# Optimization experiments

Hardware: AMD Instinct MI355X
Metric: run time of the kernel (lower is better)

The kernel has to match this reference:

```python
import jax, jax.numpy as jnp
import numpy as np

B, H, IN, OUT, T = 1024, 1024, 512, 8192, 15
EPS = 1e-5


def setup_inputs() -> dict:
    key = jax.random.key(0)
    ks = jax.random.split(key, 20)
    s = 0.02
    d = {
        'z': jax.random.normal(ks[0], (B, H), jnp.float32),
        'input_length': T,
        # ConvTranspose1d weights, torch layout [in, out, k] == jax 'IOH'
        'cw1': jax.random.normal(ks[1], (H, H, 3), jnp.float32) * s,
        'cb1': jax.random.normal(ks[2], (H,), jnp.float32) * s,
        'cw2': jax.random.normal(ks[3], (H, H, 3), jnp.float32) * s,
        'cb2': jax.random.normal(ks[4], (H,), jnp.float32) * s,
        'cw3': jax.random.normal(ks[5], (H, H, 3), jnp.float32) * s,
        'cb3': jax.random.normal(ks[6], (H,), jnp.float32) * s,
        # BatchNorm1d (eval mode: running stats)
        'bn1_g': jnp.ones((H,), jnp.float32), 'bn1_b': jnp.zeros((H,), jnp.float32),
        'bn1_m': jax.random.normal(ks[7], (H,), jnp.float32) * 0.1,
        'bn1_v': jax.random.uniform(ks[8], (H,), jnp.float32, 0.5, 1.5),
        'bn2_g': jnp.ones((H,), jnp.float32), 'bn2_b': jnp.zeros((H,), jnp.float32),
        'bn2_m': jax.random.normal(ks[9], (H,), jnp.float32) * 0.1,
        'bn2_v': jax.random.uniform(ks[10], (H,), jnp.float32, 0.5, 1.5),
        # GRUCell: weight_ih [3H, IN+H], weight_hh [3H, H]
        'w_ih': jax.random.normal(ks[11], (3 * H, IN + H), jnp.float32) * s,
        'w_hh': jax.random.normal(ks[12], (3 * H, H), jnp.float32) * s,
        'b_ih': jax.random.normal(ks[13], (3 * H,), jnp.float32) * s,
        'b_hh': jax.random.normal(ks[14], (3 * H,), jnp.float32) * s,
        # Linears (torch layout [out_features, in_features])
        'h2x_w': jax.random.normal(ks[15], (IN, H), jnp.float32) * s,
        'h2x_b': jax.random.normal(ks[16], (IN,), jnp.float32) * s,
        'dec2out_w': jax.random.normal(ks[17], (OUT, H), jnp.float32) * s,
        'dec2out_b': jnp.zeros((OUT,), jnp.float32),
        'out_w': jax.random.normal(ks[18], (OUT, H), jnp.float32) * s,
        'out_b': jnp.zeros((OUT,), jnp.float32),
    }
    return d


def _conv_t(x, w, b):
    # x: [B, C, L] ; torch ConvTranspose1d(k=3, s=2, pad=0): out L -> 2L+1
    y = jax.lax.conv_transpose(x, w, strides=(2,), padding='VALID',
                               dimension_numbers=('NCH', 'IOH', 'NCH'),
                               transpose_kernel=True)
    return y + b[None, :, None]


def _bn(x, g, bta, m, v):
    inv = g / jnp.sqrt(v + EPS)
    return (x - m[None, :, None]) * inv[None, :, None] + bta[None, :, None]


def reference(z, input_length, cw1, cb1, cw2, cb2, cw3, cb3,
              bn1_g, bn1_b, bn1_m, bn1_v, bn2_g, bn2_b, bn2_m, bn2_v,
              w_ih, w_hh, b_ih, b_hh, h2x_w, h2x_b,
              dec2out_w, dec2out_b, out_w, out_b):
    b = z.shape[0]
    # conv-transpose context: [B, H, 1] -> [B, H, 15]
    dec = z[:, :, None]
    dec = _bn(jax.nn.elu(_conv_t(dec, cw1, cb1)), bn1_g, bn1_b, bn1_m, bn1_v)
    dec = _bn(jax.nn.elu(_conv_t(dec, cw2, cb2)), bn2_g, bn2_b, bn2_m, bn2_v)
    dec = _conv_t(dec, cw3, cb3)
    dec_tbh = jnp.transpose(dec, (2, 0, 1))[:input_length]  # [T, B, H]

    inp0 = jnp.full((b, IN), float(OUT - 2), z.dtype)

    def step(carry, dec_t):
        h, inp = carry
        x = jnp.concatenate([inp, dec_t], axis=1)         # [B, IN+H]
        gi = x @ w_ih.T + b_ih
        gh = h @ w_hh.T + b_hh
        ir, iz, inn = jnp.split(gi, 3, axis=1)
        hr, hz, hn = jnp.split(gh, 3, axis=1)
        r = jax.nn.sigmoid(ir + hr)
        zg = jax.nn.sigmoid(iz + hz)
        n = jnp.tanh(inn + r * hn)
        h_new = (1.0 - zg) * n + zg * h
        inp_new = jax.nn.relu(h_new @ h2x_w.T + h2x_b)    # eval-mode branch
        return (h_new, inp_new), h_new

    (_, _), hs = jax.lax.scan(step, (z, inp0), dec_tbh)   # hs: [T, B, H]

    dec_flat = dec_tbh.reshape(-1, H)
    out_flat = hs.reshape(-1, H)
    dec_o = dec_flat @ dec2out_w.T + dec2out_b            # [T*B, OUT]
    output = out_flat @ out_w.T + out_b                   # [T*B, OUT]
    return output, dec_o
```

## Files before the change

kernel.cpp:

```cpp
#include <hip/hip_runtime.h>
#include <math.h>


#define HD    1024
#define BATCH 1024
#define IND   512
#define OUTD  8192
#define TSTEPS 15
#define EPSV  1e-5f

typedef unsigned short u16;
typedef __attribute__((ext_vector_type(8))) short bf16x8;
typedef __attribute__((ext_vector_type(8))) unsigned short u16x8;
typedef __attribute__((ext_vector_type(4))) unsigned short u16x4;
typedef __attribute__((ext_vector_type(4))) float f32x4;

__device__ __forceinline__ u16 f2b(float f) {
    union { float f; unsigned u; } x; x.f = f;
    unsigned r = x.u + 0x7fffu + ((x.u >> 16) & 1u);
    return (u16)(r >> 16);
}
__device__ __forceinline__ float b2f(u16 v) {
    union { unsigned u; float f; } x; x.u = ((unsigned)v) << 16; return x.f;
}

typedef __attribute__((address_space(1))) const void gas_t;
typedef __attribute__((address_space(3))) void las_t;
__device__ __forceinline__ void gload_lds16(const u16* g, u16* l) {
    __builtin_amdgcn_global_load_lds((gas_t*)g, (las_t*)l, 16, 0, 0);
}

template<int EPI, bool WF32, bool WB16>
__device__ __forceinline__ void gemm_tile128(
    u16* As, u16* Bs,
    int bm, int bn,
    int K1, const u16* A1, int lda1, const u16* B1, int ldb1,
    int K2, const u16* A2, int lda2, const u16* B2, int ldb2,
    const float* bias,
    const float* bng, const float* bnb, const float* bnm, const float* bnv,
    float* Cf, u16* Cb, int ldc)
{
    const int tid  = threadIdx.x;
    const int lane = tid & 63;
    const int w    = tid >> 6;
    const int wr   = w >> 1, wc = w & 1;
    const int r_in = lane >> 2;
    const int c_in = (lane & 3) * 8;

    f32x4 acc[4][4];
#pragma unroll
    for (int m = 0; m < 4; ++m)
#pragma unroll
        for (int n = 0; n < 4; ++n) acc[m][n] = (f32x4){0.f, 0.f, 0.f, 0.f};

#pragma unroll 1
    for (int pair = 0; pair < 2; ++pair) {
        const int K = pair ? K2 : K1;
        if (K == 0) continue;
        const int lda = pair ? lda2 : lda1;
        const int ldb = pair ? ldb2 : ldb1;
        const u16* Ag = (pair ? A2 : A1) + (size_t)bm * lda;
        const u16* Bg = (pair ? B2 : B1) + (size_t)bn * ldb;

        for (int k0 = 0; k0 < K; k0 += 32) {
#pragma unroll
            for (int i = 0; i < 2; ++i) {
                gload_lds16(Ag + (size_t)(i * 64 + w * 16 + r_in) * lda + k0 + c_in,
                            &As[i * 2048 + w * 512]);
                gload_lds16(Bg + (size_t)(i * 64 + w * 16 + r_in) * ldb + k0 + c_in,
                            &Bs[i * 2048 + w * 512]);
            }
            __syncthreads();

            const int fr = lane & 15;
            const int fk = (lane >> 4) * 8;
            bf16x8 av[4], bv[4];
#pragma unroll
            for (int m = 0; m < 4; ++m)
                av[m] = *(const bf16x8*)&As[(wr * 64 + m * 16 + fr) * 32 + fk];
#pragma unroll
            for (int n = 0; n < 4; ++n)
                bv[n] = *(const bf16x8*)&Bs[(wc * 64 + n * 16 + fr) * 32 + fk];
#pragma unroll
            for (int m = 0; m < 4; ++m)
#pragma unroll
                for (int n = 0; n < 4; ++n)
                    acc[m][n] = __builtin_amdgcn_mfma_f32_16x16x32_bf16(
                                    av[m], bv[n], acc[m][n], 0, 0, 0);
            __syncthreads();
        }
    }

    const int col_l = lane & 15;
    const int row_h = (lane >> 4) * 4;
#pragma unroll
    for (int m = 0; m < 4; ++m) {
#pragma unroll
        for (int j = 0; j < 4; ++j) {
            const int row = bm + wr * 64 + m * 16 + row_h + j;
#pragma unroll
            for (int n = 0; n < 4; ++n) {
                const int col = bn + wc * 64 + n * 16 + col_l;
                float v = acc[m][n][j] + bias[col];
                if (EPI == 1) {
                    float e = v > 0.f ? v : expm1f(v);
                    float sc = bng[col] * rsqrtf(bnv[col] + EPSV);
                    v = (e - bnm[col]) * sc + bnb[col];
                }
                if (WF32) Cf[(size_t)row * ldc + col] = v;
                if (WB16) Cb[(size_t)row * ldc + col] = f2b(v);
            }
        }
    }
}

__device__ __forceinline__ void proj_rider(u16* sm, int g,
    const u16* A, const u16* B, const float* bias, float* C)
{
    gemm_tile128<0, true, false>(sm, sm + 4096,
        (g >> 6) * 128, (g & 63) * 128,
        HD, A, HD, B, HD, 0, nullptr, 0, nullptr, 0,
        bias, nullptr, nullptr, nullptr, nullptr, C, nullptr, OUTD);
}

__device__ __forceinline__ void gdec_rider(u16* sm, int t, int g,
    const u16* dec3b, const u16* wihb, const float* b_ih, u16* gdecb)
{
    const int row = g / 24, col = g - row * 24;
    gemm_tile128<0, false, true>(sm, sm + 4096,
        row * 128, col * 128,
        HD, dec3b + (size_t)t * BATCH * HD, HD, wihb + IND, IND + HD,
        0, nullptr, 0, nullptr, 0,
        b_ih, nullptr, nullptr, nullptr, nullptr,
        nullptr, gdecb + (size_t)t * BATCH * 3 * HD, 3 * HD);
}

__launch_bounds__(256)
__global__ void gdec_head(const u16* __restrict__ dec3b, const u16* __restrict__ wihb,
                          const float* __restrict__ b_ih, u16* __restrict__ gdecb)
{
    __shared__ __align__(16) u16 sm[8192];
    const int bid = blockIdx.x;
    if (bid < 192) gdec_rider(sm, 0, bid, dec3b, wihb, b_ih, gdecb);
    else           gdec_rider(sm, 1, bid - 192, dec3b, wihb, b_ih, gdecb);
}

template<int EPI>
__launch_bounds__(256)
__global__ void conv_gemm(int Lin, const u16* X, const u16* W, const float* bias,
                          const float* bng, const float* bnb, const float* bnm, const float* bnv,
                          u16* Y)
{
    __shared__ __align__(16) u16 sm[8192];
    const int t = blockIdx.z;
    int l0 = 0, k0 = 0, l1 = 0, k1 = 0, cnt = 0;
    for (int l = 0; l < Lin; ++l) {
        int k = t - 2 * l;
        if (k >= 0 && k < 3) { if (!cnt) { l0 = l; k0 = k; } else { l1 = l; k1 = k; } ++cnt; }
    }
    const size_t BH = (size_t)BATCH * HD, HH = (size_t)HD * HD;
    gemm_tile128<EPI, false, true>(sm, sm + 4096,
        blockIdx.y * 128, blockIdx.x * 128,
        HD, X + l0 * BH, HD, W + k0 * HH, HD,
        cnt > 1 ? HD : 0, X + l1 * BH, HD, W + k1 * HH, HD,
        bias, bng, bnb, bnm, bnv, nullptr, Y + (size_t)t * BH, HD);
}

#define KTILE(Ag, lda_, Bg, ldb_, k0_, ACC2)                                      \
  {                                                                               \
    const int k0 = (k0_);                                                         \
    gload_lds16((Ag) + (size_t)(tid >> 2) * (lda_) + k0 + (tid & 3) * 8,          \
                &As[tid * 8]);                                                    \
    _Pragma("unroll")                                                             \
    for (int i_ = 0; i_ < 3; ++i_) {                                              \
      const int u_ = tid + i_ * 256;                                              \
      gload_lds16((Bg) + (size_t)((u_ >> 8) * HD + bn + ((u_ & 255) >> 2)) * (ldb_)\
                       + k0 + (u_ & 3) * 8,                                       \
                  &Bs[u_ * 8]);                                                   \
    }                                                                             \
    __syncthreads();                                                              \
    {                                                                             \
      bf16x8 av0 = *(const bf16x8*)&As[(wr * 32 + fr) * 32 + fk];                 \
      bf16x8 av1 = *(const bf16x8*)&As[(wr * 32 + 16 + fr) * 32 + fk];            \
      _Pragma("unroll")                                                           \
      for (int n_ = 0; n_ < 2; ++n_) {                                            \
        const int bo = (wc * 32 + n_ * 16 + fr) * 32 + fk;                        \
        bf16x8 bv = *(const bf16x8*)&Bs[bo];                                      \
        ar[0][n_] = __builtin_amdgcn_mfma_f32_16x16x32_bf16(av0, bv, ar[0][n_], 0, 0, 0); \
        ar[1][n_] = __builtin_amdgcn_mfma_f32_16x16x32_bf16(av1, bv, ar[1][n_], 0, 0, 0); \
        bv = *(const bf16x8*)&Bs[2048 + bo];                                      \
        az[0][n_] = __builtin_amdgcn_mfma_f32_16x16x32_bf16(av0, bv, az[0][n_], 0, 0, 0); \
        az[1][n_] = __builtin_amdgcn_mfma_f32_16x16x32_bf16(av1, bv, az[1][n_], 0, 0, 0); \
        bv = *(const bf16x8*)&Bs[4096 + bo];                                      \
        ACC2[0][n_] = __builtin_amdgcn_mfma_f32_16x16x32_bf16(av0, bv, ACC2[0][n_], 0, 0, 0); \
        ACC2[1][n_] = __builtin_amdgcn_mfma_f32_16x16x32_bf16(av1, bv, ACC2[1][n_], 0, 0, 0); \
      }                                                                           \
    }                                                                             \
    __syncthreads();                                                              \
  }

__launch_bounds__(256)
__global__ void gih_cell(int t,
    const u16* __restrict__ inpb,  const u16* __restrict__ wih,
    const u16* __restrict__ hbp,   const u16* __restrict__ whh,
    const u16* __restrict__ gdecb, const float* __restrict__ extra0,
    const float* __restrict__ b_hh, const float* __restrict__ hp,
    float* __restrict__ hf, u16* __restrict__ hsbt,
    const u16* __restrict__ dec3b, const u16* __restrict__ d2owb,
    const float* __restrict__ d2ob, float* __restrict__ out1,
    const float* __restrict__ b_ih)
{
    __shared__ __align__(16) u16 sm[8192];
    const int bid = blockIdx.x;
    const int tid = threadIdx.x, l = tid & 63, w = tid >> 6;
    const int wr = w >> 1, wc = w & 1;
    const int fr = l & 15, fk = (l >> 4) * 8;

    if (bid >= 256) {
        int rid = bid - 256;
        if (t <= 12) {
            if (rid < 192) {
                gdec_rider(sm, t + 2, rid, dec3b, wih, b_ih, (u16*)gdecb);
                return;
            }
            rid -= 192;
        }
        proj_rider(sm, t * 512 + rid, dec3b, d2owb, d2ob, out1);
        return;
    }

    u16* As = sm;
    u16* Bs = sm + 2048;
    const int bm = (bid >> 4) * 64;
    const int bn = (bid & 15) * 64;

    f32x4 ar[2][2], az[2][2], ain[2][2], ahn[2][2];
#pragma unroll
    for (int m = 0; m < 2; ++m)
#pragma unroll
        for (int n = 0; n < 2; ++n) {
            ar[m][n] = (f32x4){0.f, 0.f, 0.f, 0.f};
            az[m][n] = (f32x4){0.f, 0.f, 0.f, 0.f};
            ain[m][n] = (f32x4){0.f, 0.f, 0.f, 0.f};
            ahn[m][n] = (f32x4){0.f, 0.f, 0.f, 0.f};
        }

    const u16* Ah = hbp + (size_t)bm * HD;
    const u16* Ai = inpb + (size_t)bm * IND;
    for (int kt = 0; kt < 32; ++kt)
        KTILE(Ah, HD, whh, HD, kt * 32, ahn);
    if (t > 0)
        for (int kt = 0; kt < 16; ++kt)
            KTILE(Ai, IND, wih, (IND + HD), kt * 32, ain);

    const u16* gdect = gdecb + (size_t)t * BATCH * 3 * HD;
    const int rh = (l >> 4) * 4;
#pragma unroll
    for (int m = 0; m < 2; ++m)
#pragma unroll
        for (int n = 0; n < 2; ++n)
#pragma unroll
            for (int j = 0; j < 4; ++j) {
                const int R = bm + wr * 32 + m * 16 + rh + j;
                const int C = bn + wc * 32 + n * 16 + fr;
                const size_t g3 = (size_t)R * (3 * HD);
                float gr  = ar[m][n][j] + b2f(gdect[g3 + C])      + b_hh[C];
                float gz  = az[m][n][j] + b2f(gdect[g3 + HD + C]) + b_hh[HD + C];
                float gin = ain[m][n][j] + b2f(gdect[g3 + 2 * HD + C]);
                float ghn = ahn[m][n][j] + b_hh[2 * HD + C];
                if (extra0) {
                    gr  += extra0[C];
                    gz  += extra0[HD + C];
                    gin += extra0[2 * HD + C];
                }
                const float rg = 1.f / (1.f + expf(-gr));
                const float zg = 1.f / (1.f + expf(-gz));
                const float nn = tanhf(gin + rg * ghn);
                const float h  = (1.f - zg) * nn + zg * hp[(size_t)R * HD + C];
                hf[(size_t)R * HD + C] = h;
                hsbt[(size_t)R * HD + C] = f2b(h);
            }
}

__launch_bounds__(256)
__global__ void h2x_k(int t,
    const u16* __restrict__ hbp, const u16* __restrict__ wx,
    const float* __restrict__ xb, u16* __restrict__ inp,
    const u16* __restrict__ hsb, const u16* __restrict__ outwb,
    const float* __restrict__ outb, float* __restrict__ out0)
{
    __shared__ __align__(16) u16 sm[8192];
    const int bid = blockIdx.x;
    const int tid = threadIdx.x, l = tid & 63, w = tid >> 6;
    const int wr = w >> 1, wc = w & 1;
    const int fr = l & 15, fk = (l >> 4) * 8;

    if (bid >= 128) {
        proj_rider(sm, (t - 1) * 512 + (bid - 128), hsb, outwb, outb, out0);
        return;
    }

    u16* As = sm;
    u16* Bs = sm + 2048;
    const int bm = (bid >> 3) * 64;
    const int bn = (bid & 7) * 64;

    f32x4 acc[2][2];
#pragma unroll
    for (int m = 0; m < 2; ++m)
#pragma unroll
        for (int n = 0; n < 2; ++n) acc[m][n] = (f32x4){0.f, 0.f, 0.f, 0.f};
    const u16* Ag = hbp + (size_t)bm * HD;
    const u16* Bg = wx + (size_t)bn * HD;
    for (int kt = 0; kt < 32; ++kt) {
        const int k0 = kt * 32;
        gload_lds16(Ag + (size_t)(tid >> 2) * HD + k0 + (tid & 3) * 8, &As[tid * 8]);
        gload_lds16(Bg + (size_t)(tid >> 2) * HD + k0 + (tid & 3) * 8, &Bs[tid * 8]);
        __syncthreads();
        bf16x8 av0 = *(const bf16x8*)&As[(wr * 32 + fr) * 32 + fk];
        bf16x8 av1 = *(const bf16x8*)&As[(wr * 32 + 16 + fr) * 32 + fk];
#pragma unroll
        for (int n = 0; n < 2; ++n) {
            bf16x8 bv = *(const bf16x8*)&Bs[(wc * 32 + n * 16 + fr) * 32 + fk];
            acc[0][n] = __builtin_amdgcn_mfma_f32_16x16x32_bf16(av0, bv, acc[0][n], 0, 0, 0);
            acc[1][n] = __builtin_amdgcn_mfma_f32_16x16x32_bf16(av1, bv, acc[1][n], 0, 0, 0);
        }
        __syncthreads();
    }
    const int rh = (l >> 4) * 4;
#pragma unroll
    for (int m = 0; m < 2; ++m)
#pragma unroll
        for (int n = 0; n < 2; ++n)
#pragma unroll
            for (int j = 0; j < 4; ++j) {
                const int R = bm + wr * 32 + m * 16 + rh + j;
                const int C = bn + wc * 32 + n * 16 + fr;
                inp[(size_t)R * IND + C] = f2b(fmaxf(acc[m][n][j] + xb[C], 0.f));
            }
}

__launch_bounds__(256)
__global__ void proj_k(int g0, const u16* __restrict__ A, const u16* __restrict__ B,
                       const float* __restrict__ bias, float* __restrict__ C)
{
    __shared__ __align__(16) u16 sm[8192];
    proj_rider(sm, g0 + blockIdx.x, A, B, bias, C);
}

__global__ void pack_w3(const float* __restrict__ c1, const float* __restrict__ c2,
                        const float* __restrict__ c3, u16* __restrict__ p1,
                        u16* __restrict__ p2, u16* __restrict__ p3)
{
    __shared__ float lds[768];
    const float* cw = blockIdx.y == 0 ? c1 : (blockIdx.y == 1 ? c2 : c3);
    u16* wp = blockIdx.y == 0 ? p1 : (blockIdx.y == 1 ? p2 : p3);
    const int o = blockIdx.x, t = threadIdx.x;
    const float* src = cw + (size_t)o * (HD * 3);
    for (int i0 = 0; i0 < HD; i0 += 256) {
#pragma unroll
        for (int r = 0; r < 3; ++r) lds[t + 256 * r] = src[i0 * 3 + t + 256 * r];
        __syncthreads();
#pragma unroll
        for (int k = 0; k < 3; ++k)
            wp[(size_t)k * HD * HD + (size_t)o * HD + i0 + t] = f2b(lds[t * 3 + k]);
        __syncthreads();
    }
}

__global__ void cvt_all(const float* s0, u16* d0, int n0,
                        const float* s1, u16* d1, int n1,
                        const float* s2, u16* d2, int n2,
                        const float* s3, u16* d3, int n3,
                        const float* s4, u16* d4, int n4,
                        const float* s5, u16* d5, int n5)
{
    const float* s; u16* d; int n;
    switch (blockIdx.y) {
        case 0:  s = s0; d = d0; n = n0; break;
        case 1:  s = s1; d = d1; n = n1; break;
        case 2:  s = s2; d = d2; n = n2; break;
        case 3:  s = s3; d = d3; n = n3; break;
        case 4:  s = s4; d = d4; n = n4; break;
        default: s = s5; d = d5; n = n5; break;
    }
    int i = (blockIdx.x * 256 + threadIdx.x) * 8;
    if (i >= n) return;
    float4 a = *(const float4*)(s + i);
    float4 b = *(const float4*)(s + i + 4);
    u16x8 o;
    o[0] = f2b(a.x); o[1] = f2b(a.y); o[2] = f2b(a.z); o[3] = f2b(a.w);
    o[4] = f2b(b.x); o[5] = f2b(b.y); o[6] = f2b(b.z); o[7] = f2b(b.w);
    *(u16x8*)(d + i) = o;
}

__global__ void ext0_k(const float* __restrict__ w_ih, float* __restrict__ e0)
{
    const int j = blockIdx.x, lane = threadIdx.x;
    float s = 0.f;
    for (int k = lane; k < IND; k += 64) s += w_ih[(size_t)j * (IND + HD) + k];
    for (int off = 32; off; off >>= 1) s += __shfl_down(s, off);
    if (lane == 0) e0[j] = 8190.f * s;
}

extern "C" void kernel_launch(void* const* d_in, const int* in_sizes, int n_in,
                              void* d_out, int out_size, void* d_ws, size_t ws_size,
                              hipStream_t stream)
{
    (void)in_sizes; (void)n_in; (void)out_size; (void)ws_size;

    const float* z    = (const float*)d_in[0];
    const float* cw1  = (const float*)d_in[2];
    const float* cb1  = (const float*)d_in[3];
    const float* cw2  = (const float*)d_in[4];
    const float* cb2  = (const float*)d_in[5];
    const float* cw3  = (const float*)d_in[6];
    const float* cb3  = (const float*)d_in[7];
    const float* bn1g = (const float*)d_in[8];
    const float* bn1b = (const float*)d_in[9];
    const float* bn1m = (const float*)d_in[10];
    const float* bn1v = (const float*)d_in[11];
    const float* bn2g = (const float*)d_in[12];
    const float* bn2b = (const float*)d_in[13];
    const float* bn2m = (const float*)d_in[14];
    const float* bn2v = (const float*)d_in[15];
    const float* w_ih = (const float*)d_in[16];
    const float* w_hh = (const float*)d_in[17];
    const float* b_ih = (const float*)d_in[18];
    const float* b_hh = (const float*)d_in[19];
    const float* h2xw = (const float*)d_in[20];
    const float* h2xb = (const float*)d_in[21];
    const float* d2ow = (const float*)d_in[22];
    const float* d2ob = (const float*)d_in[23];
    const float* outw = (const float*)d_in[24];
    const float* outb = (const float*)d_in[25];

    const size_t HH = (size_t)HD * HD, BH = (size_t)BATCH * HD;
    const size_t B3H = (size_t)BATCH * 3 * HD;

    u16* wsb = (u16*)d_ws;
    size_t off = 0;
    auto A16 = [&](size_t n) { u16* p = wsb + off; off += n; return p; };
    u16* wp1   = A16(3 * HH);
    u16* wp2   = A16(3 * HH);
    u16* wp3   = A16(3 * HH);
    u16* wihb  = A16((size_t)3 * HD * (IND + HD));
    u16* whhb  = A16(3 * HH);
    u16* h2xbw = A16((size_t)IND * HD);
    u16* outwb = A16((size_t)OUTD * HD);
    u16* d2owb = A16((size_t)OUTD * HD);
    u16* zb    = A16(BH);
    u16* decab = A16(3 * BH);
    u16* decbb = A16(7 * BH);
    u16* dec3b = A16(15 * BH);
    u16* hsb   = A16(15 * BH);
    u16* inpb  = A16((size_t)BATCH * IND);
    u16* gdecb = A16((size_t)TSTEPS * B3H);
    float* wsf = (float*)(wsb + ((off + 1) & ~(size_t)1));
    size_t foff = 0;
    auto A32 = [&](size_t n) { float* p = wsf + foff; foff += n; return p; };
    float* h0f   = A32(BH);
    float* h1f   = A32(BH);
    float* extra0= A32(3 * HD);

    pack_w3<<<dim3(HD, 3), 256, 0, stream>>>(cw1, cw2, cw3, wp1, wp2, wp3);
    cvt_all<<<dim3(4096, 6), 256, 0, stream>>>(
        z, zb, (int)BH,
        w_ih, wihb, 3 * HD * (IND + HD),
        w_hh, whhb, (int)(3 * HH),
        h2xw, h2xbw, IND * HD,
        outw, outwb, OUTD * HD,
        d2ow, d2owb, OUTD * HD);
    ext0_k<<<3 * HD, 64, 0, stream>>>(w_ih, extra0);

    conv_gemm<1><<<dim3(8, 8, 3), 256, 0, stream>>>(1, zb, wp1, cb1,
        bn1g, bn1b, bn1m, bn1v, decab);
    conv_gemm<1><<<dim3(8, 8, 7), 256, 0, stream>>>(3, decab, wp2, cb2,
        bn2g, bn2b, bn2m, bn2v, decbb);
    conv_gemm<0><<<dim3(8, 8, 15), 256, 0, stream>>>(7, decbb, wp3, cb3,
        nullptr, nullptr, nullptr, nullptr, dec3b);

    gdec_head<<<384, 256, 0, stream>>>(dec3b, wihb, b_ih, gdecb);

    float* out0 = (float*)d_out;
    float* out1 = out0 + (size_t)TSTEPS * BATCH * OUTD;
    for (int t = 0; t < TSTEPS; ++t) {
        const u16* hbp   = t ? hsb + (size_t)(t - 1) * BH : zb;
        const float* hpf = (t == 0) ? z : (((t - 1) & 1) ? h1f : h0f);
        float* hwf = (t & 1) ? h1f : h0f;
        if (t > 0)
            h2x_k<<<640, 256, 0, stream>>>(t, hbp, h2xbw, h2xb, inpb,
                hsb, outwb, outb, out0);
        const int ggrid = (t <= 12) ? 960 : 768;
        gih_cell<<<ggrid, 256, 0, stream>>>(t,
            inpb, wihb, hbp, whhb, gdecb,
            t ? nullptr : extra0, b_hh, hpf, hwf, hsb + (size_t)t * BH,
            dec3b, d2owb, d2ob, out1, b_ih);
    }
    proj_k<<<512, 256, 0, stream>>>(14 * 512, hsb, outwb, outb, out0);
}
```

Before: 1.486 ms.

## Double-buffer LDS tiles in GRU gate and h2x GEMM loops

Replaces the load-sync-compute-sync K loop in the gih_cell and h2x_k kernels with a two-stage LDS ping-pong. The next K tile's global-to-LDS loads are issued before the current tile's MFMAs, with explicit vmcnt waits and raw s_barrier. The goal is to hide global load latency inside these per-timestep recurrent kernels. It doubles shared memory for those blocks, which may lower occupancy for the rider blocks that share the kernel, and it relies on manual waitcnt counts being correct.

```diff
diff --git a/kernel.cpp b/kernel.cpp
--- a/kernel.cpp
+++ b/kernel.cpp
@@ -166,37 +166,25 @@
         bias, bng, bnb, bnm, bnv, nullptr, Y + (size_t)t * BH, HD);
 }
 
-#define KTILE(Ag, lda_, Bg, ldb_, k0_, ACC2)                                      \
+#define GIH_MMA(TGT)                                                              \
   {                                                                               \
-    const int k0 = (k0_);                                                         \
-    gload_lds16((Ag) + (size_t)(tid >> 2) * (lda_) + k0 + (tid & 3) * 8,          \
-                &As[tid * 8]);                                                    \
+    const u16* as = &As[buf * 2048];                                              \
+    const u16* bs = &Bs[buf * 6144];                                              \
+    bf16x8 av0 = *(const bf16x8*)&as[(wr * 32 + fr) * 32 + fk];                   \
+    bf16x8 av1 = *(const bf16x8*)&as[(wr * 32 + 16 + fr) * 32 + fk];              \
     _Pragma("unroll")                                                             \
-    for (int i_ = 0; i_ < 3; ++i_) {                                              \
-      const int u_ = tid + i_ * 256;                                              \
-      gload_lds16((Bg) + (size_t)((u_ >> 8) * HD + bn + ((u_ & 255) >> 2)) * (ldb_)\
-                       + k0 + (u_ & 3) * 8,                                       \
-                  &Bs[u_ * 8]);                                                   \
+    for (int n_ = 0; n_ < 2; ++n_) {                                              \
+      const int bo = (wc * 32 + n_ * 16 + fr) * 32 + fk;                          \
+      bf16x8 bv = *(const bf16x8*)&bs[bo];                                        \
+      ar[0][n_] = __builtin_amdgcn_mfma_f32_16x16x32_bf16(av0, bv, ar[0][n_], 0, 0, 0); \
+      ar[1][n_] = __builtin_amdgcn_mfma_f32_16x16x32_bf16(av1, bv, ar[1][n_], 0, 0, 0); \
+      bv = *(const bf16x8*)&bs[2048 + bo];                                        \
+      az[0][n_] = __builtin_amdgcn_mfma_f32_16x16x32_bf16(av0, bv, az[0][n_], 0, 0, 0); \
+      az[1][n_] = __builtin_amdgcn_mfma_f32_16x16x32_bf16(av1, bv, az[1][n_], 0, 0, 0); \
+      bv = *(const bf16x8*)&bs[4096 + bo];                                        \
+      TGT[0][n_] = __builtin_amdgcn_mfma_f32_16x16x32_bf16(av0, bv, TGT[0][n_], 0, 0, 0); \
+      TGT[1][n_] = __builtin_amdgcn_mfma_f32_16x16x32_bf16(av1, bv, TGT[1][n_], 0, 0, 0); \
     }                                                                             \
-    __syncthreads();                                                              \
-    {                                                                             \
-      bf16x8 av0 = *(const bf16x8*)&As[(wr * 32 + fr) * 32 + fk];                 \
-      bf16x8 av1 = *(const bf16x8*)&As[(wr * 32 + 16 + fr) * 32 + fk];            \
-      _Pragma("unroll")                                                           \
-      for (int n_ = 0; n_ < 2; ++n_) {                                            \
-        const int bo = (wc * 32 + n_ * 16 + fr) * 32 + fk;                        \
-        bf16x8 bv = *(const bf16x8*)&Bs[bo];                                      \
-        ar[0][n_] = __builtin_amdgcn_mfma_f32_16x16x32_bf16(av0, bv, ar[0][n_], 0, 0, 0); \
-        ar[1][n_] = __builtin_amdgcn_mfma_f32_16x16x32_bf16(av1, bv, ar[1][n_], 0, 0, 0); \
-        bv = *(const bf16x8*)&Bs[2048 + bo];                                      \
-        az[0][n_] = __builtin_amdgcn_mfma_f32_16x16x32_bf16(av0, bv, az[0][n_], 0, 0, 0); \
-        az[1][n_] = __builtin_amdgcn_mfma_f32_16x16x32_bf16(av1, bv, az[1][n_], 0, 0, 0); \
-        bv = *(const bf16x8*)&Bs[4096 + bo];                                      \
-        ACC2[0][n_] = __builtin_amdgcn_mfma_f32_16x16x32_bf16(av0, bv, ACC2[0][n_], 0, 0, 0); \
-        ACC2[1][n_] = __builtin_amdgcn_mfma_f32_16x16x32_bf16(av1, bv, ACC2[1][n_], 0, 0, 0); \
-      }                                                                           \
-    }                                                                             \
-    __syncthreads();                                                              \
   }
 
 __launch_bounds__(256)
@@ -210,7 +198,7 @@
     const float* __restrict__ d2ob, float* __restrict__ out1,
     const float* __restrict__ b_ih)
 {
-    __shared__ __align__(16) u16 sm[8192];
+    __shared__ __align__(16) u16 sm[16384];
     const int bid = blockIdx.x;
     const int tid = threadIdx.x, l = tid & 63, w = tid >> 6;
     const int wr = w >> 1, wc = w & 1;
@@ -230,7 +218,7 @@
     }
 
     u16* As = sm;
-    u16* Bs = sm + 2048;
+    u16* Bs = sm + 4096;
     const int bm = (bid >> 4) * 64;
     const int bn = (bid & 15) * 64;
 
@@ -247,11 +235,37 @@
 
     const u16* Ah = hbp + (size_t)bm * HD;
     const u16* Ai = inpb + (size_t)bm * IND;
-    for (int kt = 0; kt < 32; ++kt)
-        KTILE(Ah, HD, whh, HD, kt * 32, ahn);
-    if (t > 0)
-        for (int kt = 0; kt < 16; ++kt)
-            KTILE(Ai, IND, wih, (IND + HD), kt * 32, ain);
+    const int NT = (t > 0) ? 48 : 32;
+
+    auto stage = [&](int buf, int idx) {
+        const u16* Ag; int lda; const u16* Bg; int ldb; int k0;
+        if (idx < 32) { Ag = Ah; lda = HD;  Bg = whh; ldb = HD;       k0 = idx * 32; }
+        else          { Ag = Ai; lda = IND; Bg = wih; ldb = IND + HD; k0 = (idx - 32) * 32; }
+        gload_lds16(Ag + (size_t)(tid >> 2) * lda + k0 + (tid & 3) * 8,
+                    &As[buf * 2048 + tid * 8]);
+#pragma unroll
+        for (int i_ = 0; i_ < 3; ++i_) {
+            const int u_ = tid + i_ * 256;
+            gload_lds16(Bg + (size_t)((u_ >> 8) * HD + bn + ((u_ & 255) >> 2)) * ldb
+                           + k0 + (u_ & 3) * 8,
+                        &Bs[buf * 6144 + u_ * 8]);
+        }
+    };
+
+    stage(0, 0);
+#pragma unroll 1
+    for (int idx = 0; idx < NT; ++idx) {
+        const int buf = idx & 1;
+        if (idx + 1 < NT) {
+            stage(buf ^ 1, idx + 1);
+            asm volatile("s_waitcnt vmcnt(4)" ::: "memory");
+        } else {
+            asm volatile("s_waitcnt vmcnt(0)" ::: "memory");
+        }
+        __builtin_amdgcn_s_barrier();
+        if (idx < 32) { GIH_MMA(ahn); } else { GIH_MMA(ain); }
+        __builtin_amdgcn_s_barrier();
+    }
 
     const u16* gdect = gdecb + (size_t)t * BATCH * 3 * HD;
     const int rh = (l >> 4) * 4;
@@ -301,7 +315,7 @@
     }
 
     u16* As = sm;
-    u16* Bs = sm + 2048;
+    u16* Bs = sm + 4096;
     const int bm = (bid >> 3) * 64;
     const int bn = (bid & 7) * 64;
 
@@ -312,20 +326,37 @@
         for (int n = 0; n < 2; ++n) acc[m][n] = (f32x4){0.f, 0.f, 0.f, 0.f};
     const u16* Ag = hbp + (size_t)bm * HD;
     const u16* Bg = wx + (size_t)bn * HD;
+
+    auto stage = [&](int buf, int kt) {
+        const int k0 = kt * 32;
+        gload_lds16(Ag + (size_t)(tid >> 2) * HD + k0 + (tid & 3) * 8,
+                    &As[buf * 2048 + tid * 8]);
+        gload_lds16(Bg + (size_t)(tid >> 2) * HD + k0 + (tid & 3) * 8,
+                    &Bs[buf * 2048 + tid * 8]);
+    };
+
+    stage(0, 0);
+#pragma unroll 1
     for (int kt = 0; kt < 32; ++kt) {
-        const int k0 = kt * 32;
-        gload_lds16(Ag + (size_t)(tid >> 2) * HD + k0 + (tid & 3) * 8, &As[tid * 8]);
-        gload_lds16(Bg + (size_t)(tid >> 2) * HD + k0 + (tid & 3) * 8, &Bs[tid * 8]);
-        __syncthreads();
-        bf16x8 av0 = *(const bf16x8*)&As[(wr * 32 + fr) * 32 + fk];
-        bf16x8 av1 = *(const bf16x8*)&As[(wr * 32 + 16 + fr) * 32 + fk];
+        const int buf = kt & 1;
+        if (kt + 1 < 32) {
+            stage(buf ^ 1, kt + 1);
+            asm volatile("s_waitcnt vmcnt(2)" ::: "memory");
+        } else {
+            asm volatile("s_waitcnt vmcnt(0)" ::: "memory");
+        }
+        __builtin_amdgcn_s_barrier();
+        const u16* as = &As[buf * 2048];
+        const u16* bs = &Bs[buf * 2048];
+        bf16x8 av0 = *(const bf16x8*)&as[(wr * 32 + fr) * 32 + fk];
+        bf16x8 av1 = *(const bf16x8*)&as[(wr * 32 + 16 + fr) * 32 + fk];
 #pragma unroll
         for (int n = 0; n < 2; ++n) {
-            bf16x8 bv = *(const bf16x8*)&Bs[(wc * 32 + n * 16 + fr) * 32 + fk];
+            bf16x8 bv = *(const bf16x8*)&bs[(wc * 32 + n * 16 + fr) * 32 + fk];
             acc[0][n] = __builtin_amdgcn_mfma_f32_16x16x32_bf16(av0, bv, acc[0][n], 0, 0, 0);
             acc[1][n] = __builtin_amdgcn_mfma_f32_16x16x32_bf16(av1, bv, acc[1][n], 0, 0, 0);
         }
-        __syncthreads();
+        __builtin_amdgcn_s_barrier();
     }
     const int rh = (l >> 4) * 4;
 #pragma unroll
```

After: 1.521 ms. 1.02x slower.
